# Kernel optimization log

Measured on AMD Instinct MI355X. Metric: run time of the kernel, lower is better.

The kernel has to match this reference:

```python
import jax, jax.numpy as jnp
import numpy as np

B, T = 32, 128
V, E, H = 32000, 512, 1024
SOS_IDX = 1


def setup_inputs() -> dict:
    key = jax.random.key(0)
    ks = jax.random.split(key, 9)
    s = lambda n: 1.0 / np.sqrt(n)
    return {
        "target": jax.random.randint(ks[0], (B, T), 0, V, dtype=jnp.int64),
        "h0": jax.random.normal(ks[1], (B, H), dtype=jnp.float32),
        "emb": jax.random.normal(ks[2], (V, E), dtype=jnp.float32),
        "W_ih": jax.random.normal(ks[3], (H, E), dtype=jnp.float32) * s(E),
        "b_ih": jax.random.normal(ks[4], (H,), dtype=jnp.float32) * s(E),
        "W_hh": jax.random.normal(ks[5], (H, H), dtype=jnp.float32) * s(H),
        "b_hh": jax.random.normal(ks[6], (H,), dtype=jnp.float32) * s(H),
        "W_out": jax.random.normal(ks[7], (V, H), dtype=jnp.float32) * s(H),
        "b_out": jax.random.normal(ks[8], (V,), dtype=jnp.float32) * s(H),
    }


def reference(target, h0, emb, W_ih, b_ih, W_hh, b_hh, W_out, b_out):
    # Teacher-forcing ratio fixed at 1.0 (deterministic): input tokens are
    # [sos, target[:,1], ..., target[:,T-1]] per the original `target[:, t+1]`.
    Bb, Tt = target.shape
    sos = jnp.full((Bb, 1), SOS_IDX, dtype=target.dtype)
    tokens = jnp.concatenate([sos, target[:, 1:]], axis=1)  # (B, T)
    x = emb[tokens]  # (B, T, E) -- embedding gather done once, vectorized

    def step(h, x_t):
        # manual RNN cell: h' = tanh(x W_ih^T + b_ih + h W_hh^T + b_hh)
        h = jnp.tanh(x_t @ W_ih.T + b_ih + h @ W_hh.T + b_hh)  # (B, H)
        out = h @ W_out.T + b_out  # (B, V) linear decode
        return h, out

    _, outs = jax.lax.scan(step, h0, jnp.swapaxes(x, 0, 1))  # (T, B, V)
    return jnp.swapaxes(outs, 0, 1)  # (B, T, V)
```

## Files before the change

### kernel.cpp

```cpp
#include <hip/hip_runtime.h>
#include <stdint.h>

#define T_SEQ 128
#define B_SZ  32
#define H_DIM 1024
#define E_DIM 512
#define V_DIM 32000
#define SOS_TOK 1
#define NCONS 448
#define NTILES 8000

typedef float v4f __attribute__((ext_vector_type(4)));
typedef short short8 __attribute__((ext_vector_type(8)));

__device__ inline uint16_t f2bf(float x) {
    uint32_t u = __float_as_uint(x);
    uint32_t r = (u + 0x7fffu + ((u >> 16) & 1u)) >> 16;
    return (uint16_t)r;
}
__device__ inline uint32_t pack2(float a, float b) {
    return (uint32_t)f2bf(a) | ((uint32_t)f2bf(b) << 16);
}

__device__ inline void gload16(const void* g, void* l) {
    __builtin_amdgcn_global_load_lds(
        (const __attribute__((address_space(1))) uint32_t*)g,
        (__attribute__((address_space(3))) uint32_t*)l, 16, 0, 0);
}

__global__ __launch_bounds__(256) void kconv(const float* __restrict__ W,
                                             uint16_t* __restrict__ Wb) {
    size_t i = ((size_t)blockIdx.x * 256 + threadIdx.x) * 8;
    float4 a = *(const float4*)&W[i];
    float4 c = *(const float4*)&W[i + 4];
    uint4 p;
    p.x = pack2(a.x, a.y); p.y = pack2(a.z, a.w);
    p.z = pack2(c.x, c.y); p.w = pack2(c.z, c.w);
    *(uint4*)&Wb[i] = p;
}

__global__ __launch_bounds__(256) void kxwm(const int* __restrict__ target,
                                            const float* __restrict__ emb,
                                            const float* __restrict__ Wih,
                                            const float* __restrict__ bih,
                                            const float* __restrict__ bhh,
                                            float* __restrict__ xW) {
    __shared__ __align__(16) uint16_t As[128 * 32];
    __shared__ __align__(16) uint16_t Bs[128 * 32];
    __shared__ int toks[128];
    int m0 = blockIdx.x * 128, n0 = blockIdx.y * 128;
    int tid = threadIdx.x;
    if (tid < 128) {
        int row = m0 + tid;
        int t = row & (T_SEQ - 1);
        toks[tid] = (t == 0) ? SOS_TOK : target[row];
    }
    __syncthreads();

    v4f acc[4][4] = {};
    int lane = tid & 63, wv = tid >> 6, wm = wv >> 1, wn = wv & 1;
    int ar = lane & 15, ko = (lane >> 4) * 8;

    for (int k0 = 0; k0 < E_DIM; k0 += 32) {
#pragma unroll
        for (int l = 0; l < 2; ++l) {
            int c = tid + l * 256;
            int r = c >> 2, ko8 = (c & 3) * 8;
            const float* asrc = &emb[(size_t)toks[r] * E_DIM + k0 + ko8];
            float4 x = *(const float4*)asrc;
            float4 y = *(const float4*)(asrc + 4);
            uint4 p;
            p.x = pack2(x.x, x.y); p.y = pack2(x.z, x.w);
            p.z = pack2(y.x, y.y); p.w = pack2(y.z, y.w);
            *(uint4*)&As[r * 32 + ko8] = p;
            const float* bsrc = &Wih[(size_t)(n0 + r) * E_DIM + k0 + ko8];
            float4 u = *(const float4*)bsrc;
            float4 v = *(const float4*)(bsrc + 4);
            uint4 q;
            q.x = pack2(u.x, u.y); q.y = pack2(u.z, u.w);
            q.z = pack2(v.x, v.y); q.w = pack2(v.z, v.w);
            *(uint4*)&Bs[r * 32 + ko8] = q;
        }
        __syncthreads();

        short8 a[4], bfr[4];
#pragma unroll
        for (int i = 0; i < 4; ++i)
            a[i] = *(const short8*)&As[(wm * 64 + i * 16 + ar) * 32 + ko];
#pragma unroll
        for (int jj = 0; jj < 4; ++jj)
            bfr[jj] = *(const short8*)&Bs[(wn * 64 + jj * 16 + ar) * 32 + ko];
#pragma unroll
        for (int i = 0; i < 4; ++i)
#pragma unroll
            for (int jj = 0; jj < 4; ++jj)
                acc[i][jj] = __builtin_amdgcn_mfma_f32_16x16x32_bf16(
                    a[i], bfr[jj], acc[i][jj], 0, 0, 0);
        __syncthreads();
    }

    int fr = lane & 15, fq = lane >> 4;
#pragma unroll
    for (int jj = 0; jj < 4; ++jj) {
        int col = n0 + wn * 64 + jj * 16 + fr;
        float bias = bih[col] + bhh[col];
#pragma unroll
        for (int i = 0; i < 4; ++i) {
            int row = m0 + wm * 64 + i * 16 + fq * 4;
#pragma unroll
            for (int q = 0; q < 4; ++q) {
                int m = row + q;
                int b = m >> 7, t = m & (T_SEQ - 1);
                xW[((size_t)t * B_SZ + b) * H_DIM + col] = acc[i][jj][q] + bias;
            }
        }
    }
}

__global__ __launch_bounds__(256) void kfused(const uint16_t* __restrict__ hbInit,
                                              const uint16_t* __restrict__ WbHH,
                                              const float* __restrict__ xW,
                                              uint16_t* __restrict__ Hb,
                                              uint32_t* __restrict__ flags,
                                              const float* __restrict__ Wout,
                                              const float* __restrict__ bout,
                                              float* __restrict__ out) {
    __shared__ __align__(16) uint16_t As[128 * 32];
    __shared__ __align__(16) uint16_t Bs[128 * 32];
    int tid = threadIdx.x;
    int lane = tid & 63;

    if (blockIdx.x < 32) {
        __builtin_amdgcn_s_setprio(1);
        int blk = blockIdx.x;
        int bg = blk & 1, ngg = blk >> 1;
        int w = tid >> 6;
        int ncol0 = ngg * 64 + w * 16;
        int lr = lane & 15, lk = (lane >> 4) * 8;

        short8 wf[32];
        const uint16_t* wrow = WbHH + (size_t)(ncol0 + lr) * H_DIM + lk;
#pragma unroll
        for (int kt = 0; kt < 32; ++kt)
            wf[kt] = *(const short8*)(wrow + (size_t)kt * 32);

        int brow = bg * 16 + lr;
        int eb = bg * 16 + (lane >> 4) * 4;
        int en = ncol0 + lr;
        uint32_t* Hb32 = (uint32_t*)Hb;
        uint32_t* myflag = flags + (size_t)(bg * 16 + ngg) * 32;
        const uint32_t* grpflags = flags + (size_t)(bg * 16) * 32;

        for (int t = 0; t < T_SEQ; ++t) {
            const uint16_t* arow =
                ((t == 0) ? hbInit : Hb + (size_t)(t - 1) * B_SZ * H_DIM)
                + (size_t)brow * H_DIM + lk;

            float xv[4];
#pragma unroll
            for (int q = 0; q < 4; ++q)
                xv[q] = xW[((size_t)t * B_SZ + eb + q) * H_DIM + en];

            v4f ac0 = {0.f,0.f,0.f,0.f}, ac1 = {0.f,0.f,0.f,0.f};
            v4f ac2 = {0.f,0.f,0.f,0.f}, ac3 = {0.f,0.f,0.f,0.f};
            short8 af[16];
#pragma unroll
            for (int kt = 0; kt < 16; ++kt)
                af[kt] = *(const short8*)(arow + (size_t)kt * 32);
#pragma unroll
            for (int kt = 0; kt < 16; ++kt) {
                v4f* a = (kt & 3) == 0 ? &ac0 : (kt & 3) == 1 ? &ac1
                        : (kt & 3) == 2 ? &ac2 : &ac3;
                *a = __builtin_amdgcn_mfma_f32_16x16x32_bf16(af[kt], wf[kt], *a, 0, 0, 0);
            }
#pragma unroll
            for (int kt = 0; kt < 16; ++kt)
                af[kt] = *(const short8*)(arow + 512 + (size_t)kt * 32);
#pragma unroll
            for (int kt = 0; kt < 16; ++kt) {
                v4f* a = (kt & 3) == 0 ? &ac0 : (kt & 3) == 1 ? &ac1
                        : (kt & 3) == 2 ? &ac2 : &ac3;
                *a = __builtin_amdgcn_mfma_f32_16x16x32_bf16(af[kt], wf[16 + kt], *a, 0, 0, 0);
            }
            v4f acc = (ac0 + ac1) + (ac2 + ac3);

            float hv[4];
#pragma unroll
            for (int q = 0; q < 4; ++q)
                hv[q] = tanhf(acc[q] + xv[q]);

#pragma unroll
            for (int q = 0; q < 4; ++q) {
                float pv = __shfl_xor(hv[q], 1);
                bool mine = ((lane & 1) == 0) ? (q < 2) : (q >= 2);
                if (mine) {
                    uint32_t word = (lane & 1) ? pack2(pv, hv[q]) : pack2(hv[q], pv);
                    size_t i32 = (((size_t)t * B_SZ + eb + q) * H_DIM
                                  + (size_t)(en & ~1)) >> 1;
                    __hip_atomic_store(&Hb32[i32], word, __ATOMIC_RELAXED,
                                       __HIP_MEMORY_SCOPE_AGENT);
                }
            }

            __syncthreads();
            if (tid == 0)
                __hip_atomic_store(myflag, (uint32_t)(t + 1), __ATOMIC_RELEASE,
                                   __HIP_MEMORY_SCOPE_AGENT);
            if (t < T_SEQ - 1) {
                if (tid < 16) {
                    const uint32_t* f = grpflags + (size_t)tid * 32;
                    while (__hip_atomic_load(f, __ATOMIC_RELAXED,
                                             __HIP_MEMORY_SCOPE_AGENT) <= (uint32_t)t)
                        __builtin_amdgcn_s_sleep(2);
                }
                if (tid == 0)
                    (void)__hip_atomic_load(myflag, __ATOMIC_ACQUIRE,
                                            __HIP_MEMORY_SCOPE_AGENT);
                __syncthreads();
            }
        }
    } else {
        int c = blockIdx.x - 32;
        int wv = tid >> 6, wm = wv >> 1, wn = wv & 1;
        int ar = lane & 15, ko = (lane >> 4) * 8;
        int fr = lane & 15, fq = lane >> 4;
        int gate_seen = 0;

        for (int g = c; g < NTILES; g += NCONS) {
            int mtp = g / 250, nt = g - mtp * 250;
            int need = 4 * mtp + 4;
            if (need > gate_seen) {
                if (tid < 32) {
                    const uint32_t* f = flags + (size_t)tid * 32;
                    while (__hip_atomic_load(f, __ATOMIC_RELAXED,
                                             __HIP_MEMORY_SCOPE_AGENT) < (uint32_t)need)
                        __builtin_amdgcn_s_sleep(8);
                }
                __syncthreads();
                if (tid == 0)
                    (void)__hip_atomic_load(flags, __ATOMIC_ACQUIRE,
                                            __HIP_MEMORY_SCOPE_AGENT);
                __syncthreads();
                gate_seen = need;
            }

            int m0 = mtp * 128, n0 = nt * 128;
            v4f acc[4][4] = {};

            for (int k0 = 0; k0 < H_DIM; k0 += 32) {
                int wb = tid & ~63;
#pragma unroll
                for (int l = 0; l < 2; ++l) {
                    int cc = tid + l * 256;
                    int r = cc >> 2, ko8 = (cc & 3) * 8;
                    gload16(&Hb[(size_t)(m0 + r) * H_DIM + k0 + ko8],
                            (char*)As + (size_t)(wb + l * 256) * 16);
                    const float* src = &Wout[(size_t)(n0 + r) * H_DIM + k0 + ko8];
                    float4 x = *(const float4*)src;
                    float4 y = *(const float4*)(src + 4);
                    uint4 p;
                    p.x = pack2(x.x, x.y); p.y = pack2(x.z, x.w);
                    p.z = pack2(y.x, y.y); p.w = pack2(y.z, y.w);
                    *(uint4*)&Bs[r * 32 + ko8] = p;
                }
                __syncthreads();

                short8 a[4], bfr[4];
#pragma unroll
                for (int i = 0; i < 4; ++i)
                    a[i] = *(const short8*)&As[(wm * 64 + i * 16 + ar) * 32 + ko];
#pragma unroll
                for (int jj = 0; jj < 4; ++jj)
                    bfr[jj] = *(const short8*)&Bs[(wn * 64 + jj * 16 + ar) * 32 + ko];
#pragma unroll
                for (int i = 0; i < 4; ++i)
#pragma unroll
                    for (int jj = 0; jj < 4; ++jj)
                        acc[i][jj] = __builtin_amdgcn_mfma_f32_16x16x32_bf16(
                            a[i], bfr[jj], acc[i][jj], 0, 0, 0);
                __syncthreads();
            }

#pragma unroll
            for (int jj = 0; jj < 4; ++jj) {
                int col = n0 + wn * 64 + jj * 16 + fr;
                float bo = bout[col];
#pragma unroll
                for (int i = 0; i < 4; ++i) {
                    int rbase = wm * 64 + i * 16 + fq * 4;
#pragma unroll
                    for (int q = 0; q < 4; ++q) {
                        int mp = m0 + rbase + q;
                        int tt = mp >> 5, bb = mp & 31;
                        out[((size_t)bb * T_SEQ + tt) * V_DIM + col] =
                            acc[i][jj][q] + bo;
                    }
                }
            }
        }
    }
}

extern "C" void kernel_launch(void* const* d_in, const int* in_sizes, int n_in,
                              void* d_out, int out_size, void* d_ws, size_t ws_size,
                              hipStream_t stream) {
    const int*   target = (const int*)d_in[0];
    const float* h0     = (const float*)d_in[1];
    const float* emb    = (const float*)d_in[2];
    const float* Wih    = (const float*)d_in[3];
    const float* bih    = (const float*)d_in[4];
    const float* Whh    = (const float*)d_in[5];
    const float* bhh    = (const float*)d_in[6];
    const float* Wout   = (const float*)d_in[7];
    const float* bout   = (const float*)d_in[8];
    float* out = (float*)d_out;

    char* ws = (char*)d_ws;
    float*    xW     = (float*)(ws);
    uint16_t* WbHH   = (uint16_t*)(ws + 16777216);
    uint16_t* hbInit = (uint16_t*)(ws + 18874368);
    uint32_t* flags  = (uint32_t*)(ws + 18939904);
    uint16_t* Hb     = (uint16_t*)(ws + 18944000);

    kconv<<<512, 256, 0, stream>>>(Whh, WbHH);
    kconv<<<16, 256, 0, stream>>>(h0, hbInit);
    kxwm<<<dim3(32, 8), 256, 0, stream>>>(target, emb, Wih, bih, bhh, xW);
    hipMemsetAsync(flags, 0, 4096, stream);
    kfused<<<32 + NCONS, 256, 0, stream>>>(hbInit, WbHH, xW, Hb, flags,
                                           Wout, bout, out);
}
```

Measured before the change: 1.181 ms.

## Pin consumer blocks to fixed N tiles, swizzle LDS, use fast tanh

The output-projection consumers no longer stride over a flat tile list. Each of 500 consumer blocks now owns one 128-column vocab tile and a parity, and walks 16 M tiles in time order, waiting on the recurrence flags before each one. LDS loads of the H and W_out tiles use an XOR swizzle on the k-offset to avoid bank conflicts. The recurrence tanh is replaced by an exp-based approximation and the producers get higher wave priority. This shortens the serial recurrent step and balances consumer work, at the cost of slightly lower tanh precision and 500 co-resident blocks that must not starve the producers.

```diff
diff --git a/kernel.cpp b/kernel.cpp
--- a/kernel.cpp
+++ b/kernel.cpp
@@ -7,8 +7,7 @@
 #define E_DIM 512
 #define V_DIM 32000
 #define SOS_TOK 1
-#define NCONS 448
-#define NTILES 8000
+#define NCONS 500
 
 typedef float v4f __attribute__((ext_vector_type(4)));
 typedef short short8 __attribute__((ext_vector_type(8)));
@@ -20,6 +19,11 @@
 }
 __device__ inline uint32_t pack2(float a, float b) {
     return (uint32_t)f2bf(a) | ((uint32_t)f2bf(b) << 16);
+}
+
+__device__ inline float fast_tanh(float x) {
+    float e = __expf(2.0f * x);
+    return 1.0f - __fdividef(2.0f, e + 1.0f);
 }
 
 __device__ inline void gload16(const void* g, void* l) {
@@ -131,7 +135,7 @@
     int lane = tid & 63;
 
     if (blockIdx.x < 32) {
-        __builtin_amdgcn_s_setprio(1);
+        __builtin_amdgcn_s_setprio(2);
         int blk = blockIdx.x;
         int bg = blk & 1, ngg = blk >> 1;
         int w = tid >> 6;
@@ -187,7 +191,7 @@
             float hv[4];
 #pragma unroll
             for (int q = 0; q < 4; ++q)
-                hv[q] = tanhf(acc[q] + xv[q]);
+                hv[q] = fast_tanh(acc[q] + xv[q]);
 
 #pragma unroll
             for (int q = 0; q < 4; ++q) {
@@ -221,30 +225,29 @@
         }
     } else {
         int c = blockIdx.x - 32;
+        int nt = c >> 1, par = c & 1;
+        int n0 = nt * 128;
         int wv = tid >> 6, wm = wv >> 1, wn = wv & 1;
         int ar = lane & 15, ko = (lane >> 4) * 8;
+        int sx = ((ar >> 1) & 3) << 3;
         int fr = lane & 15, fq = lane >> 4;
-        int gate_seen = 0;
-
-        for (int g = c; g < NTILES; g += NCONS) {
-            int mtp = g / 250, nt = g - mtp * 250;
+
+        for (int k = 0; k < 16; ++k) {
+            int mtp = 2 * k + par;
             int need = 4 * mtp + 4;
-            if (need > gate_seen) {
-                if (tid < 32) {
-                    const uint32_t* f = flags + (size_t)tid * 32;
-                    while (__hip_atomic_load(f, __ATOMIC_RELAXED,
-                                             __HIP_MEMORY_SCOPE_AGENT) < (uint32_t)need)
-                        __builtin_amdgcn_s_sleep(8);
-                }
-                __syncthreads();
-                if (tid == 0)
-                    (void)__hip_atomic_load(flags, __ATOMIC_ACQUIRE,
-                                            __HIP_MEMORY_SCOPE_AGENT);
-                __syncthreads();
-                gate_seen = need;
-            }
-
-            int m0 = mtp * 128, n0 = nt * 128;
+            if (tid < 32) {
+                const uint32_t* f = flags + (size_t)tid * 32;
+                while (__hip_atomic_load(f, __ATOMIC_RELAXED,
+                                         __HIP_MEMORY_SCOPE_AGENT) < (uint32_t)need)
+                    __builtin_amdgcn_s_sleep(8);
+            }
+            __syncthreads();
+            if (tid == 0)
+                (void)__hip_atomic_load(flags, __ATOMIC_ACQUIRE,
+                                        __HIP_MEMORY_SCOPE_AGENT);
+            __syncthreads();
+
+            int m0 = mtp * 128;
             v4f acc[4][4] = {};
 
             for (int k0 = 0; k0 < H_DIM; k0 += 32) {
@@ -252,26 +255,27 @@
 #pragma unroll
                 for (int l = 0; l < 2; ++l) {
                     int cc = tid + l * 256;
-                    int r = cc >> 2, ko8 = (cc & 3) * 8;
-                    gload16(&Hb[(size_t)(m0 + r) * H_DIM + k0 + ko8],
+                    int r = cc >> 2;
+                    int gsw = (((cc & 3) ^ ((cc >> 3) & 3))) * 8;
+                    gload16(&Hb[(size_t)(m0 + r) * H_DIM + k0 + gsw],
                             (char*)As + (size_t)(wb + l * 256) * 16);
-                    const float* src = &Wout[(size_t)(n0 + r) * H_DIM + k0 + ko8];
+                    const float* src = &Wout[(size_t)(n0 + r) * H_DIM + k0 + gsw];
                     float4 x = *(const float4*)src;
                     float4 y = *(const float4*)(src + 4);
                     uint4 p;
                     p.x = pack2(x.x, x.y); p.y = pack2(x.z, x.w);
                     p.z = pack2(y.x, y.y); p.w = pack2(y.z, y.w);
-                    *(uint4*)&Bs[r * 32 + ko8] = p;
+                    *(uint4*)&Bs[(size_t)cc * 8] = p;
                 }
                 __syncthreads();
 
                 short8 a[4], bfr[4];
 #pragma unroll
                 for (int i = 0; i < 4; ++i)
-                    a[i] = *(const short8*)&As[(wm * 64 + i * 16 + ar) * 32 + ko];
+                    a[i] = *(const short8*)&As[(wm * 64 + i * 16 + ar) * 32 + (ko ^ sx)];
 #pragma unroll
                 for (int jj = 0; jj < 4; ++jj)
-                    bfr[jj] = *(const short8*)&Bs[(wn * 64 + jj * 16 + ar) * 32 + ko];
+                    bfr[jj] = *(const short8*)&Bs[(wn * 64 + jj * 16 + ar) * 32 + (ko ^ sx)];
 #pragma unroll
                 for (int i = 0; i < 4; ++i)
 #pragma unroll
```

Result: slower. 1.662 ms (+40.7%).

## Pre-convert W_out to bf16 and load B tiles via direct LDS loads with XOR swizzle

Applied to the files above, without the earlier changes.

Adds a conversion pass that writes W_out as bf16 into the workspace. The fused consumer then loads B tiles straight into LDS with 16-byte global-to-LDS loads instead of reading fp32 and packing in registers. An XOR swizzle on the k-offset is applied to both A and B tiles to reduce LDS bank conflicts on the fragment reads. This cuts repeated fp32 W_out traffic and per-tile conversion work, since each W_out tile is reused across 32 m-tiles, at the cost of an extra conversion kernel and about 64MB of workspace. The new path runs only if the workspace is large enough.

```diff
diff --git a/kernel.cpp b/kernel.cpp
--- a/kernel.cpp
+++ b/kernel.cpp
@@ -117,12 +117,13 @@
     }
 }
 
+template <bool BBF>
 __global__ __launch_bounds__(256) void kfused(const uint16_t* __restrict__ hbInit,
                                               const uint16_t* __restrict__ WbHH,
                                               const float* __restrict__ xW,
                                               uint16_t* __restrict__ Hb,
                                               uint32_t* __restrict__ flags,
-                                              const float* __restrict__ Wout,
+                                              const void* __restrict__ Bop,
                                               const float* __restrict__ bout,
                                               float* __restrict__ out) {
     __shared__ __align__(16) uint16_t As[128 * 32];
@@ -223,8 +224,12 @@
         int c = blockIdx.x - 32;
         int wv = tid >> 6, wm = wv >> 1, wn = wv & 1;
         int ar = lane & 15, ko = (lane >> 4) * 8;
+        int sx = BBF ? (((ar >> 1) & 3) << 3) : 0;
         int fr = lane & 15, fq = lane >> 4;
         int gate_seen = 0;
+
+        const uint16_t* Bb = (const uint16_t*)Bop;
+        const float*    Bf = (const float*)Bop;
 
         for (int g = c; g < NTILES; g += NCONS) {
             int mtp = g / 250, nt = g - mtp * 250;
@@ -249,29 +254,42 @@
 
             for (int k0 = 0; k0 < H_DIM; k0 += 32) {
                 int wb = tid & ~63;
-#pragma unroll
-                for (int l = 0; l < 2; ++l) {
-                    int cc = tid + l * 256;
-                    int r = cc >> 2, ko8 = (cc & 3) * 8;
-                    gload16(&Hb[(size_t)(m0 + r) * H_DIM + k0 + ko8],
-                            (char*)As + (size_t)(wb + l * 256) * 16);
-                    const float* src = &Wout[(size_t)(n0 + r) * H_DIM + k0 + ko8];
-                    float4 x = *(const float4*)src;
-                    float4 y = *(const float4*)(src + 4);
-                    uint4 p;
-                    p.x = pack2(x.x, x.y); p.y = pack2(x.z, x.w);
-                    p.z = pack2(y.x, y.y); p.w = pack2(y.z, y.w);
-                    *(uint4*)&Bs[r * 32 + ko8] = p;
+                if constexpr (BBF) {
+#pragma unroll
+                    for (int l = 0; l < 2; ++l) {
+                        int cc = tid + l * 256;
+                        int r = cc >> 2;
+                        int gsw = ((cc & 3) ^ ((cc >> 3) & 3)) * 8;
+                        gload16(&Hb[(size_t)(m0 + r) * H_DIM + k0 + gsw],
+                                (char*)As + (size_t)(wb + l * 256) * 16);
+                        gload16(&Bb[(size_t)(n0 + r) * H_DIM + k0 + gsw],
+                                (char*)Bs + (size_t)(wb + l * 256) * 16);
+                    }
+                } else {
+#pragma unroll
+                    for (int l = 0; l < 2; ++l) {
+                        int cc = tid + l * 256;
+                        int r = cc >> 2, ko8 = (cc & 3) * 8;
+                        gload16(&Hb[(size_t)(m0 + r) * H_DIM + k0 + ko8],
+                                (char*)As + (size_t)(wb + l * 256) * 16);
+                        const float* src = &Bf[(size_t)(n0 + r) * H_DIM + k0 + ko8];
+                        float4 x = *(const float4*)src;
+                        float4 y = *(const float4*)(src + 4);
+                        uint4 p;
+                        p.x = pack2(x.x, x.y); p.y = pack2(x.z, x.w);
+                        p.z = pack2(y.x, y.y); p.w = pack2(y.z, y.w);
+                        *(uint4*)&Bs[r * 32 + ko8] = p;
+                    }
                 }
                 __syncthreads();
 
                 short8 a[4], bfr[4];
 #pragma unroll
                 for (int i = 0; i < 4; ++i)
-                    a[i] = *(const short8*)&As[(wm * 64 + i * 16 + ar) * 32 + ko];
+                    a[i] = *(const short8*)&As[(wm * 64 + i * 16 + ar) * 32 + (ko ^ sx)];
 #pragma unroll
                 for (int jj = 0; jj < 4; ++jj)
-                    bfr[jj] = *(const short8*)&Bs[(wn * 64 + jj * 16 + ar) * 32 + ko];
+                    bfr[jj] = *(const short8*)&Bs[(wn * 64 + jj * 16 + ar) * 32 + (ko ^ sx)];
 #pragma unroll
                 for (int i = 0; i < 4; ++i)
 #pragma unroll
@@ -321,11 +339,20 @@
     uint16_t* hbInit = (uint16_t*)(ws + 18874368);
     uint32_t* flags  = (uint32_t*)(ws + 18939904);
     uint16_t* Hb     = (uint16_t*)(ws + 18944000);
+    uint16_t* WbOut  = (uint16_t*)(ws + 27332608);
+    const bool wbok = ws_size >= 92868608ull;
 
     kconv<<<512, 256, 0, stream>>>(Whh, WbHH);
     kconv<<<16, 256, 0, stream>>>(h0, hbInit);
     kxwm<<<dim3(32, 8), 256, 0, stream>>>(target, emb, Wih, bih, bhh, xW);
     hipMemsetAsync(flags, 0, 4096, stream);
-    kfused<<<32 + NCONS, 256, 0, stream>>>(hbInit, WbHH, xW, Hb, flags,
-                                           Wout, bout, out);
-}
+
+    if (wbok) {
+        kconv<<<16000, 256, 0, stream>>>(Wout, WbOut);
+        kfused<true><<<32 + NCONS, 256, 0, stream>>>(hbInit, WbHH, xW, Hb, flags,
+                                                     (const void*)WbOut, bout, out);
+    } else {
+        kfused<false><<<32 + NCONS, 256, 0, stream>>>(hbInit, WbHH, xW, Hb, flags,
+                                                      (const void*)Wout, bout, out);
+    }
+}
```

Measured after the change: 1.192 ms. Within noise of the previous version (+0.9%).
